# Performance work log

Measured on AMD Instinct MI355X. Metric: run time of the kernel, lower is better.

The kernel has to match this reference:

```python
import jax, jax.numpy as jnp
from jax import lax
import numpy as np

COMMITMENT_COST = 0.25
N_EMBED = 512
EDIM = 32


def _conv(x, w, b, stride, pad):
    # x: NCHW, w: OIHW (torch Conv2d layout)
    y = lax.conv_general_dilated(x, w, (stride, stride), [(pad, pad), (pad, pad)],
                                 dimension_numbers=("NCHW", "OIHW", "NCHW"))
    return y + b[None, :, None, None]


def _conv_t(x, w, b, stride, pad):
    # torch ConvTranspose2d weight layout: (in, out, kH, kW)
    k = w.shape[2]
    w_ = jnp.flip(w, (2, 3)).transpose(1, 0, 2, 3)  # -> OIHW
    p = k - 1 - pad
    y = lax.conv_general_dilated(x, w_, (1, 1), [(p, p), (p, p)],
                                 lhs_dilation=(stride, stride),
                                 dimension_numbers=("NCHW", "OIHW", "NCHW"))
    return y + b[None, :, None, None]


def setup_inputs() -> dict:
    key = jax.random.key(0)
    ks = jax.random.split(key, 9)
    rn = lambda k, s: jax.random.normal(k, s, jnp.float32) * 0.05
    return {
        "x": jax.random.normal(ks[0], (32, 3, 256, 256), jnp.float32),
        "e_w1": rn(ks[1], (64, 3, 4, 4)),    "e_b1": jnp.zeros((64,), jnp.float32),
        "e_w2": rn(ks[2], (128, 64, 4, 4)),  "e_b2": jnp.zeros((128,), jnp.float32),
        "e_w3": rn(ks[3], (32, 128, 3, 3)),  "e_b3": jnp.zeros((32,), jnp.float32),
        "embed": jax.random.uniform(ks[4], (N_EMBED, EDIM), jnp.float32,
                                    -1.0 / N_EMBED, 1.0 / N_EMBED),
        "d_w1": rn(ks[5], (32, 128, 3, 3)),  "d_b1": jnp.zeros((128,), jnp.float32),
        "d_w2": rn(ks[6], (128, 64, 4, 4)),  "d_b2": jnp.zeros((64,), jnp.float32),
        "d_w3": rn(ks[7], (64, 3, 4, 4)),    "d_b3": jnp.zeros((3,), jnp.float32),
    }


def reference(x, e_w1, e_b1, e_w2, e_b2, e_w3, e_b3, embed,
              d_w1, d_b1, d_w2, d_b2, d_w3, d_b3):
    # ---- encoder ----
    h = jax.nn.relu(_conv(x, e_w1, e_b1, 2, 1))   # [B,64,128,128]
    h = jax.nn.relu(_conv(h, e_w2, e_b2, 2, 1))   # [B,128,64,64]
    z = jax.nn.relu(_conv(h, e_w3, e_b3, 1, 1))   # [B,32,64,64]
    # ---- vector quantizer ----
    zp = z.transpose(0, 2, 3, 1)                  # BHWC
    zf = zp.reshape(-1, EDIM)                     # [N, 32]
    d = (zf ** 2).sum(1, keepdims=True) + (embed ** 2).sum(1) \
        - 2.0 * zf @ embed.T                      # [N, n_embed]
    idx = jnp.argmin(d, axis=1)                   # [N]
    z_q = embed[idx].reshape(zp.shape)            # gather == onehot @ embed
    sg = lax.stop_gradient
    loss = jnp.mean((sg(z_q) - zp) ** 2) + COMMITMENT_COST * jnp.mean((z_q - sg(zp)) ** 2)
    z_q_st = zp + sg(z_q - zp)                    # straight-through
    z_q_st = z_q_st.transpose(0, 3, 1, 2)         # back to NCHW
    # ---- decoder ----
    h = jax.nn.relu(_conv_t(z_q_st, d_w1, d_b1, 1, 1))  # [B,128,64,64]
    h = jax.nn.relu(_conv_t(h, d_w2, d_b2, 2, 1))       # [B,64,128,128]
    x_recon = _conv_t(h, d_w3, d_b3, 2, 1)              # [B,3,256,256]
    return x_recon, loss
```

## Files before the change

### kernel.cpp

```cpp
#include <hip/hip_runtime.h>


typedef __attribute__((ext_vector_type(8))) short     short8;
typedef __attribute__((ext_vector_type(4))) short     s16x4;
typedef __attribute__((ext_vector_type(8))) __bf16    bf16x8;
typedef __attribute__((ext_vector_type(4))) float     f32x4;
typedef __attribute__((ext_vector_type(4))) unsigned  uint32x4;

#define BATCH 32

__device__ __forceinline__ float b2f(unsigned short b) {
  union { unsigned u; float f; } v; v.u = ((unsigned)b) << 16; return v.f;
}
__device__ __forceinline__ unsigned short f2b(float f) {
  union { float f; unsigned u; } v; v.f = f;
  unsigned r = v.u + 0x7FFF + ((v.u >> 16) & 1);
  return (unsigned short)(r >> 16);
}

__global__ __launch_bounds__(256) void prep1v_k(const float* __restrict__ w,
                                                unsigned short* __restrict__ wq) {
  const int i = blockIdx.x*256 + threadIdx.x;
  const int j = i & 7, l = (i >> 3) & 63, ni = (i >> 9) & 3, ks = i >> 11;
  const int k = ks*32 + (l >> 4)*8 + j;
  const int co = ni*16 + (l & 15);
  wq[i] = (k < 48) ? f2b(w[co*48 + k]) : (unsigned short)0;
}
__global__ __launch_bounds__(256) void prep2v_k(const float* __restrict__ w,
                                                unsigned short* __restrict__ wq) {
  const int i = blockIdx.x*256 + threadIdx.x;
  const int j = i & 7, l = (i >> 3) & 63, ni = (i >> 9) & 7, ks = i >> 12;
  const int lm = l & 15, lk = l >> 4;
  const int tap = ks >> 1, cc = ks & 1;
  const int co = ni*16 + lm, ci = cc*32 + lk*8 + j;
  wq[i] = f2b(w[(co*64 + ci)*16 + tap]);
}
__global__ __launch_bounds__(256) void prep3_k(const float* __restrict__ w,
                                               unsigned short* __restrict__ wq) {
  const int i = blockIdx.x*256 + threadIdx.x;
  const int ci = i & 127, co = (i >> 7) & 31, t = i >> 12;
  wq[i] = f2b(w[(co*128 + ci)*9 + t]);
}
__global__ __launch_bounds__(256) void prep4_k(const float* __restrict__ w,
                                               unsigned short* __restrict__ wq) {
  const int i = blockIdx.x*256 + threadIdx.x;
  const int ci = i & 31, co = (i >> 5) & 127, t = i >> 12;
  wq[i] = f2b(w[(ci*128 + co)*9 + (8 - t)]);
}
__global__ __launch_bounds__(256) void prep5v_k(const float* __restrict__ w,
                                                unsigned short* __restrict__ wq) {
  const int i = blockIdx.x*256 + threadIdx.x;
  const int j = i & 7, l = (i >> 3) & 63, ni = (i >> 9) & 3;
  const int ks = (i >> 11) & 15, p = i >> 15;
  const int lm = l & 15, lk = l >> 4;
  const int py = p >> 1, px = p & 1;
  const int a = ks >> 3, b = (ks >> 2) & 1, cc = ks & 3;
  const int co = ni*16 + lm, ci = cc*32 + lk*8 + j;
  const int ky = 3 - 2*a - py, kx = 3 - 2*b - px;
  wq[i] = f2b(w[(ci*64 + co)*16 + ky*4 + kx]);
}
__global__ __launch_bounds__(256) void prep6_k(const float* __restrict__ w,
                                               unsigned short* __restrict__ wq) {
  const int i = blockIdx.x*256 + threadIdx.x;
  const int j = i & 7, l = (i >> 3) & 63, kc = (i >> 9) & 7, p = i >> 12;
  const int lm = l & 15, lk = l >> 4;
  const int a = kc >> 2, b = (kc >> 1) & 1, ch = kc & 1;
  const int ci = ch*32 + lk*8 + j, co = lm;
  const int py = p >> 1, px = p & 1;
  const int ky = 2 - 2*a + (1 - py), kx = 2 - 2*b + (1 - px);
  wq[i] = (co < 3) ? f2b(w[(ci*3 + co)*16 + ky*4 + kx]) : (unsigned short)0;
}

template<int CIN,int COUT,int HIN,int S,int KW,int NTAPS,int OSTRIDE,int P,
         bool PARITY,bool RELU,bool INF32,bool OUTF32>
__global__ __launch_bounds__(256) void mconv_k(const void* __restrict__ in_,
    const unsigned short* __restrict__ wq_, const float* __restrict__ bias,
    void* __restrict__ out_) {
  constexpr int NF  = COUT / 16;
  constexpr int NCH = CIN / 32;
  __shared__ short Al[128*40];
  __shared__ short Bl[COUT*40];
  int py = 0, px = 0, PY = P, PX = P;
  const unsigned short* wq = wq_;
  if (PARITY) {
    py = blockIdx.y >> 1; px = blockIdx.y & 1;
    PY = 1 - py; PX = 1 - px;
    wq += blockIdx.y * (NTAPS*COUT*CIN);
  }
  const int m0 = blockIdx.x * 128;
  const int w  = threadIdx.x >> 6, l = threadIdx.x & 63;
  const int lm = l & 15, lk = l >> 4;
  f32x4 acc[2][NF];
  #pragma unroll
  for (int mi = 0; mi < 2; ++mi)
    #pragma unroll
    for (int ni = 0; ni < NF; ++ni) acc[mi][ni] = (f32x4)0.0f;

  for (int tap = 0; tap < NTAPS; ++tap) {
    const int ky = tap / KW, kx = tap % KW;
    for (int ch = 0; ch < NCH; ++ch) {
      const int c0 = ch * 32;
      __syncthreads();
      for (int s = threadIdx.x; s < 512; s += 256) {
        const int row = s >> 2, part = s & 3;
        const int m = m0 + row;
        const int n = m >> 12, oy = (m >> 6) & 63, ox = m & 63;
        const int iy = oy*S - PY + ky, ix = ox*S - PX + kx;
        short8 v = (short8)(short)0;
        if (iy >= 0 && iy < HIN && ix >= 0 && ix < HIN) {
          const int base = ((n*HIN + iy)*HIN + ix)*CIN + c0 + part*8;
          if (INF32) {
            const float* pf = (const float*)in_ + base;
            const f32x4 f0 = *(const f32x4*)pf;
            const f32x4 f1 = *(const f32x4*)(pf + 4);
            #pragma unroll
            for (int j = 0; j < 4; ++j) {
              v[j]     = (short)f2b(f0[j]);
              v[j + 4] = (short)f2b(f1[j]);
            }
          } else {
            v = *(const short8*)((const unsigned short*)in_ + base);
          }
        }
        *(short8*)&Al[row*40 + part*8] = v;
      }
      for (int s = threadIdx.x; s < COUT*4; s += 256) {
        const int co = s >> 2, part = s & 3;
        *(short8*)&Bl[co*40 + part*8] =
            *(const short8*)(wq + (tap*COUT + co)*CIN + c0 + part*8);
      }
      __syncthreads();
      short8 av[2];
      #pragma unroll
      for (int mi = 0; mi < 2; ++mi)
        av[mi] = *(const short8*)&Al[(w*32 + mi*16 + lm)*40 + lk*8];
      #pragma unroll
      for (int ni = 0; ni < NF; ++ni) {
        const short8 bv = *(const short8*)&Bl[(ni*16 + lm)*40 + lk*8];
        #pragma unroll
        for (int mi = 0; mi < 2; ++mi)
          acc[mi][ni] = __builtin_amdgcn_mfma_f32_16x16x32_bf16(
              __builtin_bit_cast(bf16x8, av[mi]),
              __builtin_bit_cast(bf16x8, bv),
              acc[mi][ni], 0, 0, 0);
      }
    }
  }
  #pragma unroll
  for (int ni = 0; ni < NF; ++ni) {
    const int co = ni*16 + lm;
    const float bv = bias[co];
    #pragma unroll
    for (int mi = 0; mi < 2; ++mi) {
      #pragma unroll
      for (int r = 0; r < 4; ++r) {
        const int ml = w*32 + mi*16 + lk*4 + r;
        const int m  = m0 + ml;
        float vv = acc[mi][ni][r] + bv;
        if (RELU) vv = fmaxf(vv, 0.f);
        int off;
        if (OSTRIDE == 1) {
          off = m*COUT + co;
        } else {
          const int n = m >> 12, oy = (m >> 6) & 63, ox = m & 63;
          off = ((n*128 + oy*2 + py)*128 + ox*2 + px)*COUT + co;
        }
        if (OUTF32) ((float*)out_)[off] = vv;
        else ((unsigned short*)out_)[off] = f2b(vv);
      }
    }
  }
}

__global__ __launch_bounds__(256) void conv1m_k(const float* __restrict__ x,
    const unsigned short* __restrict__ wv, const float* __restrict__ bias,
    unsigned short* __restrict__ out) {
  __shared__ __align__(16) short RAW[12*264];
  __shared__ __align__(16) short IC[128*64];
  const int wid = ((blockIdx.x & 7) << 9) + (blockIdx.x >> 3);
  const int q = wid & 127, n = wid >> 7;
  for (int i = threadIdx.x; i < 396; i += 256)
    *(short8*)&RAW[i*8] = (short8)(short)0;
  __syncthreads();
  for (int s = threadIdx.x; s < 768; s += 256) {
    const int g = s >> 6, seg = s & 63;
    const int ci = g >> 2, ky = g & 3;
    const int iy = 2*q - 1 + ky;
    if (iy >= 0 && iy < 256) {
      const f32x4 v = *(const f32x4*)&x[((n*3 + ci)*256 + iy)*256 + seg*4];
      s16x4 sv;
      #pragma unroll
      for (int e = 0; e < 4; ++e) sv[e] = (short)f2b(v[e]);
      *(s16x4*)&RAW[g*264 + 4 + seg*4] = sv;
    }
  }
  __syncthreads();
  for (int s = threadIdx.x; s < 1024; s += 256) {
    const int kb = s & 7, ox = s >> 3;
    short8 v = (short8)(short)0;
    if (kb < 6) {
      const unsigned* u0 = (const unsigned*)&RAW[(2*kb  )*264 + 2*ox + 2];
      const unsigned* u1 = (const unsigned*)&RAW[(2*kb+1)*264 + 2*ox + 2];
      const unsigned a0 = u0[0], a1 = u0[1], a2 = u0[2];
      const unsigned b0 = u1[0], b1 = u1[1], b2 = u1[2];
      uint32x4 uv;
      uv[0] = (a0 >> 16) | (a1 << 16);
      uv[1] = (a1 >> 16) | (a2 << 16);
      uv[2] = (b0 >> 16) | (b1 << 16);
      uv[3] = (b1 >> 16) | (b2 << 16);
      v = __builtin_bit_cast(short8, uv);
    }
    const int bo = ((ox << 7) + (kb << 4)) ^ ((ox & 7) << 4);
    *(short8*)((char*)IC + bo) = v;
  }
  __syncthreads();
  const int w = threadIdx.x >> 6, l = threadIdx.x & 63;
  const int lm = l & 15, lk = l >> 4;
  f32x4 acc[2][4];
  #pragma unroll
  for (int mi = 0; mi < 2; ++mi)
    #pragma unroll
    for (int ni = 0; ni < 4; ++ni) acc[mi][ni] = (f32x4)0.0f;
  #pragma unroll
  for (int ks = 0; ks < 2; ++ks) {
    short8 bv[4];
    #pragma unroll
    for (int ni = 0; ni < 4; ++ni)
      bv[ni] = *(const short8*)(wv + (((ks*4 + ni)*64 + l) << 3));
    #pragma unroll
    for (int mi = 0; mi < 2; ++mi) {
      const int ox = w*32 + mi*16 + lm;
      const int bo = ((ox << 7) + (ks << 6) + (lk << 4)) ^ ((ox & 7) << 4);
      const short8 av = *(const short8*)((const char*)IC + bo);
      #pragma unroll
      for (int ni = 0; ni < 4; ++ni)
        acc[mi][ni] = __builtin_amdgcn_mfma_f32_16x16x32_bf16(
            __builtin_bit_cast(bf16x8, av),
            __builtin_bit_cast(bf16x8, bv[ni]),
            acc[mi][ni], 0, 0, 0);
    }
  }
  __syncthreads();
  #pragma unroll
  for (int mi = 0; mi < 2; ++mi)
    #pragma unroll
    for (int ni = 0; ni < 4; ++ni) {
      const int co = ni*16 + lm;
      const float bv = bias[co];
      #pragma unroll
      for (int r = 0; r < 4; ++r) {
        const int ox = w*32 + mi*16 + lk*4 + r;
        const int bo = ((ox << 7) + 2*co) ^ ((ox & 7) << 4);
        *(short*)((char*)IC + bo) = (short)f2b(fmaxf(acc[mi][ni][r] + bv, 0.f));
      }
    }
  __syncthreads();
  const long ob = ((long)(n*128 + q)) * 8192;
  for (int s = threadIdx.x; s < 1024; s += 256) {
    const int kb = s & 7, ox = s >> 3;
    const int bo = ((ox << 7) + (kb << 4)) ^ ((ox & 7) << 4);
    *(short8*)&out[ob + ox*64 + kb*8] = *(const short8*)((const char*)IC + bo);
  }
}

#define C2_LOAD(c) \
  _Pragma("unroll") \
  for (int s = 0; s < 9; ++s) { \
    st[s] = (short8)(short)0; \
    if (goff[s] >= 0) st[s] = *(const short8*)(in + goff[s] + (c)*32); \
  }
#define C2_WRITE \
  _Pragma("unroll") \
  for (int s = 0; s < 9; ++s) \
    if (lb[s] >= 0) *(short8*)((char*)IL + lb[s]) = st[s];
#define C2_COMPUTE(c) \
  _Pragma("unroll") \
  for (int t = 0; t < 16; ++t) { \
    const int ky = t >> 2, kx = t & 3; \
    const int p = 1 - (kx & 1), d = kx >> 1; \
    const short8 bv0 = *(const short8*)(wb + (t*2 + (c))*4096); \
    const short8 bv1 = *(const short8*)(wb + (t*2 + (c))*4096 + 512); \
    const char* Ab = (const char*)IL + (Bd0 + d*64); \
    const int imm0 = ((ky*2 + p)*66) << 6; \
    _Pragma("unroll") \
    for (int mi = 0; mi < 4; ++mi) { \
      const short8 av = *(const short8*)(Ab + imm0 + mi*1024); \
      acc[mi][0] = __builtin_amdgcn_mfma_f32_16x16x32_bf16( \
          __builtin_bit_cast(bf16x8, av), __builtin_bit_cast(bf16x8, bv0), \
          acc[mi][0], 0, 0, 0); \
      acc[mi][1] = __builtin_amdgcn_mfma_f32_16x16x32_bf16( \
          __builtin_bit_cast(bf16x8, av), __builtin_bit_cast(bf16x8, bv1), \
          acc[mi][1], 0, 0, 0); \
    } \
  }
__global__ __launch_bounds__(256) void conv2m_k(const unsigned short* __restrict__ in,
    const unsigned short* __restrict__ wv, const float* __restrict__ bias,
    unsigned short* __restrict__ out) {
  __shared__ short IL[8*66*32];
  const int wid = (blockIdx.x & 7)*256 + (blockIdx.x >> 3);
  const int q = wid & 63, n = wid >> 6;
  const int w = threadIdx.x >> 6, l = threadIdx.x & 63;
  const int lm = l & 15, lk = l >> 4;
  const int Bd0 = lm*64 + lk*16;
  const unsigned short* wb = wv + w*1024 + l*8;
  int goff[9], lb[9];
  #pragma unroll
  for (int s = 0; s < 9; ++s) {
    const int i = threadIdx.x + s*256;
    const int part = i & 3, e = i >> 2;
    const int idx = e % 66, rp = e / 66;
    const int r = rp >> 1, p = rp & 1;
    const int iy = 2*q - 1 + r, ix = 2*idx - p;
    const bool ok = (i < 2112) && iy >= 0 && iy < 128 && ix >= 0 && ix < 128;
    goff[s] = ok ? (((n*128 + iy)*128 + ix)*64 + part*8) : -1;
    lb[s]   = (i < 2112) ? (e*64 + part*16) : -1;
  }
  f32x4 acc[4][2];
  #pragma unroll
  for (int mi = 0; mi < 4; ++mi)
    #pragma unroll
    for (int ni = 0; ni < 2; ++ni) acc[mi][ni] = (f32x4)0.0f;
  short8 st[9];
  C2_LOAD(0); C2_WRITE;
  __syncthreads();
  C2_LOAD(1);
  C2_COMPUTE(0);
  __syncthreads();
  C2_WRITE;
  __syncthreads();
  C2_COMPUTE(1);
  #pragma unroll
  for (int mi = 0; mi < 4; ++mi)
    #pragma unroll
    for (int r = 0; r < 4; ++r) {
      const int ox = mi*16 + lk*4 + r;
      const int ob = ((n*64 + q)*64 + ox)*128;
      #pragma unroll
      for (int ni = 0; ni < 2; ++ni) {
        const int co = (w*2 + ni)*16 + lm;
        out[ob + co] = f2b(fmaxf(acc[mi][ni][r] + bias[co], 0.f));
      }
    }
}

#define CT2_LOAD(c) \
  _Pragma("unroll") \
  for (int s = 0; s < 7; ++s) { \
    st[s] = (short8)(short)0; \
    if (goff[s] >= 0) st[s] = *(const short8*)(in + goff[s] + (c)*64); \
  }
#define CT2_WRITE \
  _Pragma("unroll") \
  for (int s = 0; s < 7; ++s) \
    if (lb[s] >= 0) *(short8*)((char*)IL + lb[s]) = st[s];
#define CT2_COMPUTE(c) \
  _Pragma("unroll") \
  for (int u = 0; u < 8; ++u) { \
    const int a = u >> 2, b = (u >> 1) & 1, c1 = u & 1; \
    const int ks = (a << 3) | (b << 2) | (2*(c) + c1); \
    short8 bv[4]; \
    _Pragma("unroll") \
    for (int ni = 0; ni < 4; ++ni) \
      bv[ni] = *(const short8*)(wb + ks*2048 + ni*512); \
    const char* Ab = (const char*)IL + (pyb + Wb[b][c1]); \
    const int imm0 = a*8448; \
    _Pragma("unroll") \
    for (int mi = 0; mi < 4; ++mi) { \
      const short8 av = *(const short8*)(Ab + imm0 + mi*2048); \
      _Pragma("unroll") \
      for (int ni = 0; ni < 4; ++ni) \
        acc[mi][ni] = __builtin_amdgcn_mfma_f32_16x16x32_bf16( \
            __builtin_bit_cast(bf16x8, av), \
            __builtin_bit_cast(bf16x8, bv[ni]), \
            acc[mi][ni], 0, 0, 0); \
    } \
  }
__global__ __launch_bounds__(256) void convt2m_k(const unsigned short* __restrict__ in,
    const unsigned short* __restrict__ wv, const float* __restrict__ bias,
    unsigned short* __restrict__ out) {
  __shared__ short IL[3*66*64];
  const int wid = (blockIdx.x & 7)*256 + (blockIdx.x >> 3);
  const int q = wid & 63, n = wid >> 6;
  const int w = threadIdx.x >> 6, l = threadIdx.x & 63;
  const int py = w >> 1, px = w & 1;
  const int lm = l & 15, lk = l >> 4;
  int Wb[2][2];
  #pragma unroll
  for (int b = 0; b < 2; ++b) {
    const int e = lm + px + b;
    Wb[b][0] = (e << 7) + ((lk << 4) ^ ((e & 7) << 4));
    Wb[b][1] = Wb[b][0] ^ 0x40;
  }
  const int pyb = py * 8448;
  const unsigned short* wb = wv + w*32768 + l*8;
  int goff[7], lb[7];
  #pragma unroll
  for (int s = 0; s < 7; ++s) {
    const int i = threadIdx.x + s*256;
    const int part = i & 7, e = i >> 3;
    const int col = e % 66, r = e / 66;
    const int iy = q - 1 + r, ix = col - 1;
    const bool ok = (i < 1584) && iy >= 0 && iy < 64 && ix >= 0 && ix < 64;
    goff[s] = ok ? (((n*64 + iy)*64 + ix)*128 + part*8) : -1;
    lb[s]   = (i < 1584) ? ((e << 7) + ((part << 4) ^ ((col & 7) << 4))) : -1;
  }
  f32x4 acc[4][4];
  #pragma unroll
  for (int mi = 0; mi < 4; ++mi)
    #pragma unroll
    for (int ni = 0; ni < 4; ++ni) acc[mi][ni] = (f32x4)0.0f;
  short8 st[7];
  CT2_LOAD(0); CT2_WRITE;
  __syncthreads();
  CT2_LOAD(1);
  CT2_COMPUTE(0);
  __syncthreads();
  CT2_WRITE;
  __syncthreads();
  CT2_COMPUTE(1);
  const int oy = 2*q + py;
  #pragma unroll
  for (int mi = 0; mi < 4; ++mi)
    #pragma unroll
    for (int r = 0; r < 4; ++r) {
      const int ox = 2*(mi*16 + lk*4 + r) + px;
      const int ob = ((n*128 + oy)*128 + ox)*64;
      #pragma unroll
      for (int ni = 0; ni < 4; ++ni) {
        const int co = ni*16 + lm;
        out[ob + co] = f2b(fmaxf(acc[mi][ni][r] + bias[co], 0.f));
      }
    }
}

__global__ __launch_bounds__(256) void vqm_k(const float* __restrict__ z,
    const float* __restrict__ embed, float* __restrict__ zq,
    float* __restrict__ partial) {
  __shared__ short Be[512*40];
  __shared__ float en[512];
  __shared__ int   bidx[128];
  __shared__ float red[256];
  const int m0 = blockIdx.x * 128;
  for (int i = threadIdx.x; i < 4096; i += 256) {
    const int j = i >> 3, k0 = (i & 7) * 4;
    const f32x4 v = *(const f32x4*)&embed[j*32 + k0];
    s16x4 s;
    #pragma unroll
    for (int e = 0; e < 4; ++e) s[e] = (short)f2b(v[e]);
    *(s16x4*)&Be[j*40 + k0] = s;
  }
  __syncthreads();
  for (int j = threadIdx.x; j < 512; j += 256) {
    float s = 0.f;
    #pragma unroll
    for (int q = 0; q < 4; ++q) {
      const short8 v = *(const short8*)&Be[j*40 + q*8];
      #pragma unroll
      for (int e = 0; e < 8; ++e) {
        const float f = b2f((unsigned short)v[e]);
        s = fmaf(f, f, s);
      }
    }
    en[j] = s;
  }
  __syncthreads();
  const int w = threadIdx.x >> 6, l = threadIdx.x & 63;
  const int lm = l & 15, lk = l >> 4;
  const int rw = w * 32;
  short8 av[2];
  #pragma unroll
  for (int mi = 0; mi < 2; ++mi) {
    const float* zp = z + (long)(m0 + rw + mi*16 + lm)*32 + lk*8;
    const f32x4 f0 = *(const f32x4*)zp;
    const f32x4 f1 = *(const f32x4*)(zp + 4);
    short8 v;
    #pragma unroll
    for (int e = 0; e < 4; ++e) {
      v[e]     = (short)f2b(f0[e]);
      v[e + 4] = (short)f2b(f1[e]);
    }
    av[mi] = v;
  }
  float bd[2][4]; int bj[2][4];
  #pragma unroll
  for (int mi = 0; mi < 2; ++mi)
    #pragma unroll
    for (int r = 0; r < 4; ++r) { bd[mi][r] = 1e30f; bj[mi][r] = 0; }
  for (int nc = 0; nc < 8; ++nc) {
    f32x4 acc[2][4];
    #pragma unroll
    for (int mi = 0; mi < 2; ++mi)
      #pragma unroll
      for (int ni = 0; ni < 4; ++ni) acc[mi][ni] = (f32x4)0.0f;
    #pragma unroll
    for (int ni = 0; ni < 4; ++ni) {
      const short8 bv = *(const short8*)&Be[(nc*64 + ni*16 + lm)*40 + lk*8];
      #pragma unroll
      for (int mi = 0; mi < 2; ++mi)
        acc[mi][ni] = __builtin_amdgcn_mfma_f32_16x16x32_bf16(
            __builtin_bit_cast(bf16x8, av[mi]),
            __builtin_bit_cast(bf16x8, bv),
            acc[mi][ni], 0, 0, 0);
    }
    #pragma unroll
    for (int ni = 0; ni < 4; ++ni) {
      const int j = nc*64 + ni*16 + lm;
      const float e_n = en[j];
      #pragma unroll
      for (int mi = 0; mi < 2; ++mi)
        #pragma unroll
        for (int r = 0; r < 4; ++r) {
          const float d = fmaf(-2.f, acc[mi][ni][r], e_n);
          if (d < bd[mi][r]) { bd[mi][r] = d; bj[mi][r] = j; }
        }
    }
  }
  #pragma unroll
  for (int mi = 0; mi < 2; ++mi)
    #pragma unroll
    for (int r = 0; r < 4; ++r) {
      float d = bd[mi][r]; int j = bj[mi][r];
      #pragma unroll
      for (int off = 1; off < 16; off <<= 1) {
        const float od = __shfl_xor(d, off);
        const int   oj = __shfl_xor(j, off);
        if (od < d || (od == d && oj < j)) { d = od; j = oj; }
      }
      if (lm == 0) bidx[rw + mi*16 + lk*4 + r] = j;
    }
  __syncthreads();
  const int pl = threadIdx.x >> 1, hf = (threadIdx.x & 1) * 16;
  const int code = bidx[pl];
  const long pb = (long)(m0 + pl)*32 + hf;
  float se = 0.f;
  #pragma unroll
  for (int q = 0; q < 4; ++q) {
    const f32x4 ev = *(const f32x4*)&embed[code*32 + hf + q*4];
    const f32x4 zv = *(const f32x4*)&z[pb + q*4];
    *(f32x4*)&zq[pb + q*4] = ev;
    const f32x4 df = ev - zv;
    #pragma unroll
    for (int e = 0; e < 4; ++e) se = fmaf(df[e], df[e], se);
  }
  red[threadIdx.x] = se; __syncthreads();
  for (int s = 128; s > 0; s >>= 1) {
    if (threadIdx.x < s) red[threadIdx.x] += red[threadIdx.x + s];
    __syncthreads();
  }
  if (threadIdx.x == 0) partial[blockIdx.x] = red[0];
}

__global__ __launch_bounds__(256) void loss_k(const float* __restrict__ part,
                                              float* __restrict__ out) {
  __shared__ float red[256];
  const int t = threadIdx.x;
  float s = 0.f;
  #pragma unroll
  for (int q = 0; q < 4; ++q) s += part[t + q*256];
  red[t] = s; __syncthreads();
  for (int st = 128; st > 0; st >>= 1) {
    if (t < st) red[t] += red[t + st];
    __syncthreads();
  }
  if (t == 0) out[0] = red[0] * (1.25f / (131072.f * 32.f));
}

__global__ __launch_bounds__(256) void convt3m_k(const unsigned short* __restrict__ in,
    const unsigned short* __restrict__ wq6, const float* __restrict__ bias,
    float* __restrict__ out) {
  __shared__ short8 IL[3*8*66];
  const int h = blockIdx.x & 1, q = (blockIdx.x >> 1) & 127, n = blockIdx.x >> 8;
  for (int i = threadIdx.x; i < 1584; i += 256) {
    const int c8 = i & 7, t = i >> 3, ixl = t % 66, r = t / 66;
    const int iy = q - 1 + r, ix = h*64 - 1 + ixl;
    short8 v = (short8)(short)0;
    if (iy >= 0 && iy < 128 && ix >= 0 && ix < 128)
      v = *(const short8*)(in + (((long)(n*128 + iy)*128 + ix)*64 + c8*8));
    IL[(r*8 + c8)*66 + ixl] = v;
  }
  const int w = threadIdx.x >> 6, l = threadIdx.x & 63;
  const int py = w >> 1, px = w & 1;
  const int lm = l & 15, lk = l >> 4;
  short8 bfrag[8];
  #pragma unroll
  for (int kc = 0; kc < 8; ++kc)
    bfrag[kc] = *(const short8*)(wq6 + (((w*8 + kc)*64 + l) << 3));
  __syncthreads();
  f32x4 acc[4];
  #pragma unroll
  for (int mi = 0; mi < 4; ++mi) acc[mi] = (f32x4)0.0f;
  #pragma unroll
  for (int kc = 0; kc < 8; ++kc) {
    const int a = kc >> 2, b = (kc >> 1) & 1, ch = kc & 1;
    const int base = (((py + a)*8 + ch*4 + lk)*66) + px + b;
    #pragma unroll
    for (int mi = 0; mi < 4; ++mi) {
      const short8 av = *(const short8*)&IL[base + mi*16 + lm];
      acc[mi] = __builtin_amdgcn_mfma_f32_16x16x32_bf16(
          __builtin_bit_cast(bf16x8, av),
          __builtin_bit_cast(bf16x8, bfrag[kc]),
          acc[mi], 0, 0, 0);
    }
  }
  if (lm < 3) {
    const float bv = bias[lm];
    const int oy = 2*q + py;
    const long ob = ((long)(n*3 + lm))*65536 + oy*256;
    #pragma unroll
    for (int mi = 0; mi < 4; ++mi)
      #pragma unroll
      for (int r = 0; r < 4; ++r) {
        const int xq = mi*16 + lk*4 + r;
        out[ob + h*128 + 2*xq + px] = acc[mi][r] + bv;
      }
  }
}

extern "C" void kernel_launch(void* const* d_in, const int* in_sizes, int n_in,
                              void* d_out, int out_size, void* d_ws, size_t ws_size,
                              hipStream_t stream) {
  const float* x   = (const float*)d_in[0];
  const float* ew1 = (const float*)d_in[1];  const float* eb1 = (const float*)d_in[2];
  const float* ew2 = (const float*)d_in[3];  const float* eb2 = (const float*)d_in[4];
  const float* ew3 = (const float*)d_in[5];  const float* eb3 = (const float*)d_in[6];
  const float* emb = (const float*)d_in[7];
  const float* dw1 = (const float*)d_in[8];  const float* db1 = (const float*)d_in[9];
  const float* dw2 = (const float*)d_in[10]; const float* db2 = (const float*)d_in[11];
  const float* dw3 = (const float*)d_in[12]; const float* db3 = (const float*)d_in[13];
  float* out = (float*)d_out;

  uint8_t* w8 = (uint8_t*)d_ws;
  unsigned short* h1 = (unsigned short*)w8;
  unsigned short* h2 = (unsigned short*)(w8 + 67108864);
  float* z   = (float*)(w8 + 100663296);
  float* zq  = (float*)(w8 + 117440512);
  float* part = (float*)(w8 + 67108864);
  unsigned short* wq2 = (unsigned short*)(w8 + 117440512);
  unsigned short* wq3 = (unsigned short*)(w8 + 117440512 + 262144);
  unsigned short* wq1 = (unsigned short*)(w8 + 117440512 + 335872);
  unsigned short* wq4 = (unsigned short*)(w8 + 100663296);
  unsigned short* wq5 = (unsigned short*)(w8 + 100663296 + 73728);
  unsigned short* wq6 = (unsigned short*)(w8 + 100663296 + 335872);
  unsigned short* d1 = h2;
  unsigned short* d2 = h1;

  prep1v_k<<<dim3(16),256,0,stream>>>(ew1, wq1);
  prep2v_k<<<dim3(512),256,0,stream>>>(ew2, wq2);
  prep3_k<<<dim3(144),256,0,stream>>>(ew3, wq3);
  conv1m_k<<<dim3(4096),256,0,stream>>>(x, wq1, eb1, h1);
  conv2m_k<<<dim3(2048),256,0,stream>>>(h1, wq2, eb2, h2);
  mconv_k<128,32,64,1,3,9,1,1,false,true,false,true>
      <<<dim3(1024),256,0,stream>>>(h2, wq3, eb3, z);
  vqm_k<<<dim3(1024),256,0,stream>>>(z, emb, zq, part);
  loss_k<<<dim3(1),256,0,stream>>>(part, out + 6291456);
  prep4_k<<<dim3(144),256,0,stream>>>(dw1, wq4);
  prep5v_k<<<dim3(512),256,0,stream>>>(dw2, wq5);
  prep6_k<<<dim3(64),256,0,stream>>>(dw3, wq6);
  mconv_k<32,128,64,1,3,9,1,1,false,true,true,false>
      <<<dim3(1024),256,0,stream>>>(zq, wq4, db1, d1);
  convt2m_k<<<dim3(2048),256,0,stream>>>(d1, wq5, db2, d2);
  convt3m_k<<<dim3(8192),256,0,stream>>>(d2, wq6, db3, out);
}
```

Measured before the change: 382.2 us.

## Replace generic implicit-GEMM conv with specialized halo-tiled conv3 and deconv1 kernels

```diff
diff --git a/kernel.cpp b/kernel.cpp
--- a/kernel.cpp
+++ b/kernel.cpp
@@ -6,8 +6,6 @@
 typedef __attribute__((ext_vector_type(8))) __bf16    bf16x8;
 typedef __attribute__((ext_vector_type(4))) float     f32x4;
 typedef __attribute__((ext_vector_type(4))) unsigned  uint32x4;
-
-#define BATCH 32
 
 __device__ __forceinline__ float b2f(unsigned short b) {
   union { unsigned u; float f; } v; v.u = ((unsigned)b) << 16; return v.f;
@@ -35,17 +33,22 @@
   const int co = ni*16 + lm, ci = cc*32 + lk*8 + j;
   wq[i] = f2b(w[(co*64 + ci)*16 + tap]);
 }
-__global__ __launch_bounds__(256) void prep3_k(const float* __restrict__ w,
-                                               unsigned short* __restrict__ wq) {
+__global__ __launch_bounds__(256) void prep3v_k(const float* __restrict__ w,
+                                                unsigned short* __restrict__ wq) {
   const int i = blockIdx.x*256 + threadIdx.x;
-  const int ci = i & 127, co = (i >> 7) & 31, t = i >> 12;
-  wq[i] = f2b(w[(co*128 + ci)*9 + t]);
-}
-__global__ __launch_bounds__(256) void prep4_k(const float* __restrict__ w,
-                                               unsigned short* __restrict__ wq) {
+  const int j = i & 7, l = (i >> 3) & 63, ni = (i >> 9) & 1, ks = i >> 10;
+  const int lm = l & 15, lk = l >> 4;
+  const int tap = ks >> 2, cf = ks & 3;
+  const int co = ni*16 + lm, ci = cf*32 + lk*8 + j;
+  wq[i] = f2b(w[(co*128 + ci)*9 + tap]);
+}
+__global__ __launch_bounds__(256) void prep4v_k(const float* __restrict__ w,
+                                                unsigned short* __restrict__ wq) {
   const int i = blockIdx.x*256 + threadIdx.x;
-  const int ci = i & 31, co = (i >> 5) & 127, t = i >> 12;
-  wq[i] = f2b(w[(ci*128 + co)*9 + (8 - t)]);
+  const int j = i & 7, l = (i >> 3) & 63, ni = (i >> 9) & 7, tap = i >> 12;
+  const int lm = l & 15, lk = l >> 4;
+  const int co = ni*16 + lm, ci = lk*8 + j;
+  wq[i] = f2b(w[(ci*128 + co)*9 + (8 - tap)]);
 }
 __global__ __launch_bounds__(256) void prep5v_k(const float* __restrict__ w,
                                                 unsigned short* __restrict__ wq) {
@@ -69,107 +72,6 @@
   const int py = p >> 1, px = p & 1;
   const int ky = 2 - 2*a + (1 - py), kx = 2 - 2*b + (1 - px);
   wq[i] = (co < 3) ? f2b(w[(ci*3 + co)*16 + ky*4 + kx]) : (unsigned short)0;
-}
-
-template<int CIN,int COUT,int HIN,int S,int KW,int NTAPS,int OSTRIDE,int P,
-         bool PARITY,bool RELU,bool INF32,bool OUTF32>
-__global__ __launch_bounds__(256) void mconv_k(const void* __restrict__ in_,
-    const unsigned short* __restrict__ wq_, const float* __restrict__ bias,
-    void* __restrict__ out_) {
-  constexpr int NF  = COUT / 16;
-  constexpr int NCH = CIN / 32;
-  __shared__ short Al[128*40];
-  __shared__ short Bl[COUT*40];
-  int py = 0, px = 0, PY = P, PX = P;
-  const unsigned short* wq = wq_;
-  if (PARITY) {
-    py = blockIdx.y >> 1; px = blockIdx.y & 1;
-    PY = 1 - py; PX = 1 - px;
-    wq += blockIdx.y * (NTAPS*COUT*CIN);
-  }
-  const int m0 = blockIdx.x * 128;
-  const int w  = threadIdx.x >> 6, l = threadIdx.x & 63;
-  const int lm = l & 15, lk = l >> 4;
-  f32x4 acc[2][NF];
-  #pragma unroll
-  for (int mi = 0; mi < 2; ++mi)
-    #pragma unroll
-    for (int ni = 0; ni < NF; ++ni) acc[mi][ni] = (f32x4)0.0f;
-
-  for (int tap = 0; tap < NTAPS; ++tap) {
-    const int ky = tap / KW, kx = tap % KW;
-    for (int ch = 0; ch < NCH; ++ch) {
-      const int c0 = ch * 32;
-      __syncthreads();
-      for (int s = threadIdx.x; s < 512; s += 256) {
-        const int row = s >> 2, part = s & 3;
-        const int m = m0 + row;
-        const int n = m >> 12, oy = (m >> 6) & 63, ox = m & 63;
-        const int iy = oy*S - PY + ky, ix = ox*S - PX + kx;
-        short8 v = (short8)(short)0;
-        if (iy >= 0 && iy < HIN && ix >= 0 && ix < HIN) {
-          const int base = ((n*HIN + iy)*HIN + ix)*CIN + c0 + part*8;
-          if (INF32) {
-            const float* pf = (const float*)in_ + base;
-            const f32x4 f0 = *(const f32x4*)pf;
-            const f32x4 f1 = *(const f32x4*)(pf + 4);
-            #pragma unroll
-            for (int j = 0; j < 4; ++j) {
-              v[j]     = (short)f2b(f0[j]);
-              v[j + 4] = (short)f2b(f1[j]);
-            }
-          } else {
-            v = *(const short8*)((const unsigned short*)in_ + base);
-          }
-        }
-        *(short8*)&Al[row*40 + part*8] = v;
-      }
-      for (int s = threadIdx.x; s < COUT*4; s += 256) {
-        const int co = s >> 2, part = s & 3;
-        *(short8*)&Bl[co*40 + part*8] =
-            *(const short8*)(wq + (tap*COUT + co)*CIN + c0 + part*8);
-      }
-      __syncthreads();
-      short8 av[2];
-      #pragma unroll
-      for (int mi = 0; mi < 2; ++mi)
-        av[mi] = *(const short8*)&Al[(w*32 + mi*16 + lm)*40 + lk*8];
-      #pragma unroll
-      for (int ni = 0; ni < NF; ++ni) {
-        const short8 bv = *(const short8*)&Bl[(ni*16 + lm)*40 + lk*8];
-        #pragma unroll
-        for (int mi = 0; mi < 2; ++mi)
-          acc[mi][ni] = __builtin_amdgcn_mfma_f32_16x16x32_bf16(
-              __builtin_bit_cast(bf16x8, av[mi]),
-              __builtin_bit_cast(bf16x8, bv),
-              acc[mi][ni], 0, 0, 0);
-      }
-    }
-  }
-  #pragma unroll
-  for (int ni = 0; ni < NF; ++ni) {
-    const int co = ni*16 + lm;
-    const float bv = bias[co];
-    #pragma unroll
-    for (int mi = 0; mi < 2; ++mi) {
-      #pragma unroll
-      for (int r = 0; r < 4; ++r) {
-        const int ml = w*32 + mi*16 + lk*4 + r;
-        const int m  = m0 + ml;
-        float vv = acc[mi][ni][r] + bv;
-        if (RELU) vv = fmaxf(vv, 0.f);
-        int off;
-        if (OSTRIDE == 1) {
-          off = m*COUT + co;
-        } else {
-          const int n = m >> 12, oy = (m >> 6) & 63, ox = m & 63;
-          off = ((n*128 + oy*2 + py)*128 + ox*2 + px)*COUT + co;
-        }
-        if (OUTF32) ((float*)out_)[off] = vv;
-        else ((unsigned short*)out_)[off] = f2b(vv);
-      }
-    }
-  }
 }
 
 __global__ __launch_bounds__(256) void conv1m_k(const float* __restrict__ x,
@@ -338,6 +240,166 @@
       #pragma unroll
       for (int ni = 0; ni < 2; ++ni) {
         const int co = (w*2 + ni)*16 + lm;
+        out[ob + co] = f2b(fmaxf(acc[mi][ni][r] + bias[co], 0.f));
+      }
+    }
+}
+
+#define C3_LOAD(c) \
+  _Pragma("unroll") \
+  for (int s = 0; s < 9; ++s) { \
+    st[s] = (short8)(short)0; \
+    if (goff[s] >= 0) st[s] = *(const short8*)(in + goff[s] + (c)*64); \
+  }
+#define C3_WRITE \
+  _Pragma("unroll") \
+  for (int s = 0; s < 9; ++s) \
+    if (lb[s] >= 0) *(short8*)((char*)IL + lb[s]) = st[s];
+#define C3_COMPUTE(c) \
+  _Pragma("unroll") \
+  for (int u = 0; u < 18; ++u) { \
+    const int tap = u >> 1, cc = u & 1; \
+    const int ky = tap / 3, kx = tap % 3; \
+    const int ks = tap*4 + (c)*2 + cc; \
+    const short8 bv0 = *(const short8*)(wb + ks*1024); \
+    const short8 bv1 = *(const short8*)(wb + ks*1024 + 512); \
+    const char* Ab = (const char*)IL + (Wc[kx][cc]); \
+    const int imm0 = ky*8448; \
+    _Pragma("unroll") \
+    for (int mi = 0; mi < 2; ++mi) { \
+      const short8 av = *(const short8*)(Ab + imm0 + mi*2048); \
+      acc[mi][0] = __builtin_amdgcn_mfma_f32_16x16x32_bf16( \
+          __builtin_bit_cast(bf16x8, av), __builtin_bit_cast(bf16x8, bv0), \
+          acc[mi][0], 0, 0, 0); \
+      acc[mi][1] = __builtin_amdgcn_mfma_f32_16x16x32_bf16( \
+          __builtin_bit_cast(bf16x8, av), __builtin_bit_cast(bf16x8, bv1), \
+          acc[mi][1], 0, 0, 0); \
+    } \
+  }
+__global__ __launch_bounds__(256) void conv3m_k(const unsigned short* __restrict__ in,
+    const unsigned short* __restrict__ wv, const float* __restrict__ bias,
+    float* __restrict__ out) {
+  __shared__ short IL[4*66*64];
+  const int wid = (blockIdx.x & 7)*128 + (blockIdx.x >> 3);
+  const int q = wid & 31, n = wid >> 5;
+  const int w = threadIdx.x >> 6, l = threadIdx.x & 63;
+  const int lm = l & 15, lk = l >> 4;
+  const int row = w >> 1, oxb = (w & 1) * 32;
+  int goff[9], lb[9];
+  #pragma unroll
+  for (int s = 0; s < 9; ++s) {
+    const int i = threadIdx.x + s*256;
+    const int part = i & 7, e = i >> 3;
+    const int col = e % 66, r = e / 66;
+    const int iy = 2*q - 1 + r, ix = col - 1;
+    const bool ok = (i < 2112) && iy >= 0 && iy < 64 && ix >= 0 && ix < 64;
+    goff[s] = ok ? (((n*64 + iy)*64 + ix)*128 + part*8) : -1;
+    lb[s]   = (i < 2112) ? ((e << 7) + ((part << 4) ^ ((col & 7) << 4))) : -1;
+  }
+  int Wc[3][2];
+  #pragma unroll
+  for (int kx = 0; kx < 3; ++kx) {
+    const int e = oxb + lm + kx;
+    Wc[kx][0] = row*8448 + (e << 7) + ((lk << 4) ^ ((e & 7) << 4));
+    Wc[kx][1] = Wc[kx][0] ^ 0x40;
+  }
+  const unsigned short* wb = wv + l*8;
+  f32x4 acc[2][2];
+  #pragma unroll
+  for (int mi = 0; mi < 2; ++mi)
+    #pragma unroll
+    for (int ni = 0; ni < 2; ++ni) acc[mi][ni] = (f32x4)0.0f;
+  short8 st[9];
+  C3_LOAD(0); C3_WRITE;
+  __syncthreads();
+  C3_LOAD(1);
+  C3_COMPUTE(0);
+  __syncthreads();
+  C3_WRITE;
+  __syncthreads();
+  C3_COMPUTE(1);
+  const int oy = 2*q + row;
+  #pragma unroll
+  for (int mi = 0; mi < 2; ++mi)
+    #pragma unroll
+    for (int r = 0; r < 4; ++r) {
+      const int ox = oxb + mi*16 + lk*4 + r;
+      const long mb = ((long)((n*64 + oy)*64 + ox)) * 32;
+      #pragma unroll
+      for (int ni = 0; ni < 2; ++ni) {
+        const int co = ni*16 + lm;
+        out[mb + co] = fmaxf(acc[mi][ni][r] + bias[co], 0.f);
+      }
+    }
+}
+
+__global__ __launch_bounds__(256) void d1m_k(const float* __restrict__ in,
+    const unsigned short* __restrict__ wv, const float* __restrict__ bias,
+    unsigned short* __restrict__ out) {
+  __shared__ short IL[264*40];
+  const int wid = (blockIdx.x & 7)*128 + (blockIdx.x >> 3);
+  const int q = wid & 31, n = wid >> 5;
+  const int w = threadIdx.x >> 6, l = threadIdx.x & 63;
+  const int lm = l & 15, lk = l >> 4;
+  const int row = w >> 1, oxb = (w & 1) * 32;
+  for (int i = threadIdx.x; i < 1056; i += 256) {
+    const int part = i & 3, e = i >> 2;
+    const int col = e % 66, r = e / 66;
+    const int iy = 2*q - 1 + r, ix = col - 1;
+    short8 v = (short8)(short)0;
+    if (iy >= 0 && iy < 64 && ix >= 0 && ix < 64) {
+      const float* p = in + (((long)((n*64 + iy)*64 + ix)) * 32 + part*8);
+      const f32x4 f0 = *(const f32x4*)p;
+      const f32x4 f1 = *(const f32x4*)(p + 4);
+      #pragma unroll
+      for (int e2 = 0; e2 < 4; ++e2) {
+        v[e2]     = (short)f2b(f0[e2]);
+        v[e2 + 4] = (short)f2b(f1[e2]);
+      }
+    }
+    *(short8*)&IL[e*40 + part*8] = v;
+  }
+  const unsigned short* wb = wv + l*8;
+  int Wd[3];
+  #pragma unroll
+  for (int kx = 0; kx < 3; ++kx)
+    Wd[kx] = row*5280 + (oxb + lm + kx)*80 + lk*16;
+  __syncthreads();
+  f32x4 acc[2][8];
+  #pragma unroll
+  for (int mi = 0; mi < 2; ++mi)
+    #pragma unroll
+    for (int ni = 0; ni < 8; ++ni) acc[mi][ni] = (f32x4)0.0f;
+  #pragma unroll
+  for (int tap = 0; tap < 9; ++tap) {
+    const int ky = tap / 3, kx = tap % 3;
+    short8 bv[8];
+    #pragma unroll
+    for (int ni = 0; ni < 8; ++ni)
+      bv[ni] = *(const short8*)(wb + (tap*8 + ni)*512);
+    const char* Ab = (const char*)IL + Wd[kx];
+    const int imm0 = ky*5280;
+    #pragma unroll
+    for (int mi = 0; mi < 2; ++mi) {
+      const short8 av = *(const short8*)(Ab + imm0 + mi*1280);
+      #pragma unroll
+      for (int ni = 0; ni < 8; ++ni)
+        acc[mi][ni] = __builtin_amdgcn_mfma_f32_16x16x32_bf16(
+            __builtin_bit_cast(bf16x8, av),
+            __builtin_bit_cast(bf16x8, bv[ni]),
+            acc[mi][ni], 0, 0, 0);
+    }
+  }
+  const int oy = 2*q + row;
+  #pragma unroll
+  for (int mi = 0; mi < 2; ++mi)
+    #pragma unroll
+    for (int r = 0; r < 4; ++r) {
+      const int ox = oxb + mi*16 + lk*4 + r;
+      const int ob = ((n*64 + oy)*64 + ox)*128;
+      #pragma unroll
+      for (int ni = 0; ni < 8; ++ni) {
+        const int co = ni*16 + lm;
         out[ob + co] = f2b(fmaxf(acc[mi][ni][r] + bias[co], 0.f));
       }
     }
@@ -646,18 +708,16 @@
 
   prep1v_k<<<dim3(16),256,0,stream>>>(ew1, wq1);
   prep2v_k<<<dim3(512),256,0,stream>>>(ew2, wq2);
-  prep3_k<<<dim3(144),256,0,stream>>>(ew3, wq3);
+  prep3v_k<<<dim3(144),256,0,stream>>>(ew3, wq3);
   conv1m_k<<<dim3(4096),256,0,stream>>>(x, wq1, eb1, h1);
   conv2m_k<<<dim3(2048),256,0,stream>>>(h1, wq2, eb2, h2);
-  mconv_k<128,32,64,1,3,9,1,1,false,true,false,true>
-      <<<dim3(1024),256,0,stream>>>(h2, wq3, eb3, z);
+  conv3m_k<<<dim3(1024),256,0,stream>>>(h2, wq3, eb3, z);
   vqm_k<<<dim3(1024),256,0,stream>>>(z, emb, zq, part);
   loss_k<<<dim3(1),256,0,stream>>>(part, out + 6291456);
-  prep4_k<<<dim3(144),256,0,stream>>>(dw1, wq4);
+  prep4v_k<<<dim3(144),256,0,stream>>>(dw1, wq4);
   prep5v_k<<<dim3(512),256,0,stream>>>(dw2, wq5);
   prep6_k<<<dim3(64),256,0,stream>>>(dw3, wq6);
-  mconv_k<32,128,64,1,3,9,1,1,false,true,true,false>
-      <<<dim3(1024),256,0,stream>>>(zq, wq4, db1, d1);
+  d1m_k<<<dim3(1024),256,0,stream>>>(zq, wq4, db1, d1);
   convt2m_k<<<dim3(2048),256,0,stream>>>(d1, wq5, db2, d2);
   convt3m_k<<<dim3(8192),256,0,stream>>>(d2, wq6, db3, out);
 }
```

Measured after the change: 358.7 us. 1.07x faster.
